# Kernel tuning notes

Hardware: AMD Instinct MI355X
Metric: run time of the kernel (lower is better)

The kernel has to match this reference:

```python
import jax, jax.numpy as jnp
import numpy as np

VOCAB, EMBED = 2048, 512
N = 65536  # = batch(2048) * num_slots(8) * tokens_per_slot(4)


def setup_inputs() -> dict:
    key = jax.random.key(0)
    ks = jax.random.split(key, 6)
    return {
        "z": jax.random.normal(ks[0], (N, 64), dtype=jnp.float32),
        "emb_W": jax.random.uniform(ks[1], (VOCAB, EMBED), dtype=jnp.float32,
                                    minval=-1.0 / VOCAB, maxval=1.0 / VOCAB),
        "pre_W": jax.random.normal(ks[2], (64, EMBED), dtype=jnp.float32) * 0.125,
        "pre_b": jax.random.normal(ks[3], (EMBED,), dtype=jnp.float32) * 0.02,
        "post_W": jax.random.normal(ks[4], (EMBED, 64), dtype=jnp.float32) * 0.044,
        "post_b": jax.random.normal(ks[5], (64,), dtype=jnp.float32) * 0.02,
    }


def reference(z, emb_W, pre_W, pre_b, post_W, post_b):
    # pre_quant_conv: Linear(64 -> embed_dim)
    zp = z @ pre_W + pre_b  # [N, E]
    # squared-distance to codebook: |z|^2 + |e|^2 - 2 z.e
    d = (jnp.sum(zp * zp, axis=1, keepdims=True)
         + jnp.sum(emb_W * emb_W, axis=1)
         - 2.0 * (zp @ emb_W.T))  # [N, V]
    tokens = jnp.argmin(d, axis=-1)  # [N] int
    z_q = emb_W[tokens]  # embedding gather [N, E]
    # post_quant_conv: Linear(embed_dim -> 64)
    z_q = z_q @ post_W + post_b  # [N, 64]
    return tokens, z_q
```

## Files before the change

### kernel.cpp

```cpp
#include <hip/hip_runtime.h>

#define EN  512
#define KIN 64
#define VN  2048
#define MARGIN 2.5e-3f
#define PRUNE  2.3e-3f
#define CAP 32

typedef __attribute__((ext_vector_type(8))) short bf16x8;
typedef __attribute__((ext_vector_type(4))) float f32x4;

static __device__ inline short f2bf(float f) {
  unsigned u = __builtin_bit_cast(unsigned, f);
  unsigned r = (u + 0x7FFFu + ((u >> 16) & 1u)) >> 16;
  return (short)r;
}
static __device__ inline unsigned encg(float f) {
  unsigned u = __builtin_bit_cast(unsigned, f);
  return (u & 0x80000000u) ? ~u : (u | 0x80000000u);
}
static __device__ inline float decg(unsigned e) {
  unsigned u = (e & 0x80000000u) ? (e & 0x7FFFFFFFu) : ~e;
  return __builtin_bit_cast(float, u);
}

__global__ __launch_bounds__(256) void k_prep(const float* __restrict__ emb,
                                              const float* __restrict__ pW,
                                              const float* __restrict__ pb,
                                              float* __restrict__ t2,
                                              short* __restrict__ dst,
                                              float* __restrict__ embq) {
#pragma clang fp contract(off)
  __shared__ float xs[64][129];
  const int tid = threadIdx.x;
  if (blockIdx.x >= 32) {
    const int gid = (blockIdx.x - 32) * 256 + tid;
    const int v = gid >> 6, c = gid & 63;
    const float* er = emb + (size_t)v * EN;
    float acc = 0.f;
#pragma unroll 8
    for (int k = 0; k < EN; ++k)
      acc = fmaf(er[k], pW[(size_t)k * 64 + c], acc);
    embq[(size_t)v * 64 + c] = acc + pb[c];
    return;
  }
  const int row0 = blockIdx.x * 64;
  float s[4];
  for (int ch = 0; ch < 4; ++ch) {
    __syncthreads();
#pragma unroll
    for (int i = 0; i < 32; ++i) {
      const int l = tid + i * 256;
      xs[l >> 7][l & 127] = emb[(size_t)(row0 + (l >> 7)) * EN + ch * 128 + (l & 127)];
    }
    __syncthreads();
    if (tid < 64) {
      float r8[8];
#pragma unroll
      for (int j = 0; j < 8; ++j) { const float v = xs[tid][j]; r8[j] = v * v; }
      for (int i = 8; i < 128; i += 8) {
#pragma unroll
        for (int j = 0; j < 8; ++j) { const float v = xs[tid][i + j]; r8[j] = r8[j] + v * v; }
      }
      s[ch] = ((r8[0] + r8[1]) + (r8[2] + r8[3])) + ((r8[4] + r8[5]) + (r8[6] + r8[7]));
    }
  }
  if (tid < 64) t2[row0 + tid] = (s[0] + s[1]) + (s[2] + s[3]);
  for (int i = tid; i < 64 * 64; i += 256) {
    const int v = row0 + (i >> 6), k8 = i & 63;
    const float4 f0 = ((const float4*)emb)[(size_t)v * 128 + k8 * 2];
    const float4 f1 = ((const float4*)emb)[(size_t)v * 128 + k8 * 2 + 1];
    short4 h0, h1;
    h0.x = f2bf(f0.x); h0.y = f2bf(f0.y); h0.z = f2bf(f0.z); h0.w = f2bf(f0.w);
    h1.x = f2bf(f1.x); h1.y = f2bf(f1.y); h1.z = f2bf(f1.z); h1.w = f2bf(f1.w);
    const int vt = v >> 4, vrow = v & 15, kb = k8 >> 2, q = k8 & 3;
    const int off = ((vt * 16 + kb) * 64 + q * 16 + vrow) * 8;
    *(short4*)&dst[off] = h0;
    *(short4*)&dst[off + 4] = h1;
  }
}

__global__ __launch_bounds__(512, 4) void k_dist(const float* __restrict__ z,
                                                 const float* __restrict__ preW,
                                                 const float* __restrict__ preb,
                                                 const short* __restrict__ embhs,
                                                 const float* __restrict__ embf,
                                                 const float* __restrict__ t2,
                                                 float* __restrict__ zp,
                                                 int* __restrict__ rowcnt,
                                                 unsigned short* __restrict__ slots,
                                                 float* __restrict__ gslots,
                                                 unsigned long long* __restrict__ keys) {
#pragma clang fp contract(off)
  __shared__ short As[64 * 512];
  __shared__ unsigned rmaxs[64];
  __shared__ int cnt_s[64];
  const int tid = threadIdx.x;
  const int wave = tid >> 6, lane = tid & 63;
  const int quad = lane >> 4, l15 = lane & 15;
  const int row0 = blockIdx.x * 64;

  if (tid < 64) { rmaxs[tid] = 0u; cnt_s[tid] = 0; keys[row0 + tid] = ~0ull; }

  {
    const int rg = tid >> 5, cg = tid & 31;
    for (int ph = 0; ph < 4; ++ph) {
      const int j = ph * 128 + 4 * cg;
      f32x4 acc[4];
#pragma unroll
      for (int r = 0; r < 4; ++r) acc[r] = (f32x4){0.f, 0.f, 0.f, 0.f};
#pragma unroll 4
      for (int k4 = 0; k4 < 16; ++k4) {
        f32x4 zr[4];
#pragma unroll
        for (int r = 0; r < 4; ++r)
          zr[r] = *(const f32x4*)&z[(size_t)(row0 + 4 * rg + r) * KIN + 4 * k4];
#pragma unroll
        for (int kk = 0; kk < 4; ++kk) {
          const f32x4 w = *(const f32x4*)&preW[(size_t)(4 * k4 + kk) * EN + j];
#pragma unroll
          for (int r = 0; r < 4; ++r) {
            acc[r][0] = fmaf(zr[r][kk], w[0], acc[r][0]);
            acc[r][1] = fmaf(zr[r][kk], w[1], acc[r][1]);
            acc[r][2] = fmaf(zr[r][kk], w[2], acc[r][2]);
            acc[r][3] = fmaf(zr[r][kk], w[3], acc[r][3]);
          }
        }
      }
      const f32x4 bb = *(const f32x4*)&preb[j];
      const int kb = j >> 5, q = (j >> 3) & 3, half = ((j >> 2) & 1) * 4;
#pragma unroll
      for (int r = 0; r < 4; ++r) {
        f32x4 o;
        o[0] = acc[r][0] + bb[0]; o[1] = acc[r][1] + bb[1];
        o[2] = acc[r][2] + bb[2]; o[3] = acc[r][3] + bb[3];
        const int row = 4 * rg + r;
        *(f32x4*)&zp[(size_t)(row0 + row) * EN + j] = o;
        short4 h;
        h.x = f2bf(o[0]); h.y = f2bf(o[1]); h.z = f2bf(o[2]); h.w = f2bf(o[3]);
        const int mt = row >> 4, mrow = row & 15;
        *(short4*)&As[((mt * 16 + kb) * 64 + q * 16 + mrow) * 8 + half] = h;
      }
    }
  }
  __syncthreads();

  for (int win = 0; win < 8; ++win) {
    const int v0 = win * 256 + wave * 32;
    const int vt0 = win * 16 + wave * 2;
    const short* B0 = embhs + (((size_t)vt0 * 16) * 64 + lane) * 8;
    const short* B1 = embhs + ((((size_t)vt0 + 1) * 16) * 64 + lane) * 8;
    const float t2v0 = t2[v0 + l15];
    const float t2v1 = t2[v0 + 16 + l15];
    f32x4 acc[4][2];
#pragma unroll
    for (int mt = 0; mt < 4; ++mt) {
      acc[mt][0] = (f32x4){0.f, 0.f, 0.f, 0.f};
      acc[mt][1] = (f32x4){0.f, 0.f, 0.f, 0.f};
    }
    bf16x8 b00 = *(const bf16x8*)&B0[0];
    bf16x8 b01 = *(const bf16x8*)&B1[0];
    bf16x8 b10 = *(const bf16x8*)&B0[512];
    bf16x8 b11 = *(const bf16x8*)&B1[512];
    for (int kb = 0; kb < 16; kb += 2) {
      const int k2 = (kb + 2) & 15;
      const bf16x8 n00 = *(const bf16x8*)&B0[k2 * 512];
      const bf16x8 n01 = *(const bf16x8*)&B1[k2 * 512];
      __builtin_amdgcn_s_setprio(1);
#pragma unroll
      for (int mt = 0; mt < 4; ++mt) {
        const bf16x8 a = *(const bf16x8*)&As[((mt * 16 + kb) * 64 + lane) * 8];
        acc[mt][0] = __builtin_amdgcn_mfma_f32_16x16x32_bf16(a, b00, acc[mt][0], 0, 0, 0);
        acc[mt][1] = __builtin_amdgcn_mfma_f32_16x16x32_bf16(a, b01, acc[mt][1], 0, 0, 0);
      }
      __builtin_amdgcn_s_setprio(0);
      const int k3 = (kb + 3) & 15;
      const bf16x8 n10 = *(const bf16x8*)&B0[k3 * 512];
      const bf16x8 n11 = *(const bf16x8*)&B1[k3 * 512];
      __builtin_amdgcn_s_setprio(1);
#pragma unroll
      for (int mt = 0; mt < 4; ++mt) {
        const bf16x8 a = *(const bf16x8*)&As[((mt * 16 + kb + 1) * 64 + lane) * 8];
        acc[mt][0] = __builtin_amdgcn_mfma_f32_16x16x32_bf16(a, b10, acc[mt][0], 0, 0, 0);
        acc[mt][1] = __builtin_amdgcn_mfma_f32_16x16x32_bf16(a, b11, acc[mt][1], 0, 0, 0);
      }
      __builtin_amdgcn_s_setprio(0);
      b00 = n00; b01 = n01; b10 = n10; b11 = n11;
    }

#pragma unroll
    for (int mt = 0; mt < 4; ++mt)
#pragma unroll
      for (int r = 0; r < 4; ++r) {
        acc[mt][0][r] = fmaf(2.f, acc[mt][0][r], -t2v0);
        acc[mt][1][r] = fmaf(2.f, acc[mt][1][r], -t2v1);
      }
#pragma unroll
    for (int mt = 0; mt < 4; ++mt)
#pragma unroll
      for (int r = 0; r < 4; ++r) {
        float m = fmaxf(acc[mt][0][r], acc[mt][1][r]);
        m = fmaxf(m, __shfl_xor(m, 1, 16));
        m = fmaxf(m, __shfl_xor(m, 2, 16));
        m = fmaxf(m, __shfl_xor(m, 4, 16));
        m = fmaxf(m, __shfl_xor(m, 8, 16));
        if (l15 == 0) atomicMax(&rmaxs[mt * 16 + quad * 4 + r], encg(m));
      }
#pragma unroll
    for (int mt = 0; mt < 4; ++mt)
#pragma unroll
      for (int r = 0; r < 4; ++r) {
        const int rl = mt * 16 + quad * 4 + r;
        const float thr = decg(rmaxs[rl]) - MARGIN;
        const int grow = row0 + rl;
#pragma unroll
        for (int nt = 0; nt < 2; ++nt) {
          const float gv = acc[mt][nt][r];
          if (gv > thr) {
            const int v = v0 + nt * 16 + l15;
            const int idx = atomicAdd(&cnt_s[rl], 1);
            if (idx < CAP) {
              slots[grow * CAP + idx] = (unsigned short)v;
              gslots[grow * CAP + idx] = gv;
            } else {
              float accx = 0.f;
              const float* zr = zp + (size_t)grow * EN;
              const float* er = embf + (size_t)v * EN;
              float r8n[8], sn[4];
#pragma unroll
              for (int ch = 0; ch < 4; ++ch) {
#pragma unroll
                for (int _j = 0; _j < 8; ++_j) r8n[_j] = 0.f;
#pragma unroll 8
                for (int kk = 0; kk < 128; ++kk) {
                  const int k = ch * 128 + kk;
                  const float zv = zr[k];
                  accx = fmaf(zv, er[k], accx);
                  r8n[kk & 7] = r8n[kk & 7] + zv * zv;
                }
                sn[ch] = ((r8n[0] + r8n[1]) + (r8n[2] + r8n[3])) + ((r8n[4] + r8n[5]) + (r8n[6] + r8n[7]));
              }
              const float t1v = (sn[0] + sn[1]) + (sn[2] + sn[3]);
              const float d = (t1v + t2[v]) - 2.0f * accx;
              atomicMin(keys + grow, ((unsigned long long)encg(d) << 32) | (unsigned)v);
            }
          }
        }
      }
  }
  __syncthreads();
  if (tid < 64) rowcnt[row0 + tid] = cnt_s[tid];
}

__global__ __launch_bounds__(256) void k_tail2(const float* __restrict__ zp,
                                               const float* __restrict__ embf,
                                               const float* __restrict__ t2,
                                               const int* __restrict__ rowcnt,
                                               const unsigned short* __restrict__ slots,
                                               const float* __restrict__ gslots,
                                               unsigned long long* __restrict__ keys,
                                               const float* __restrict__ embq,
                                               float* __restrict__ tokf,
                                               float* __restrict__ out) {
#pragma clang fp contract(off)
  __shared__ int toks[64];
  __shared__ float t1s[64];
  __shared__ int wl_n;
  __shared__ unsigned wl_s[64 * CAP];
  __shared__ __align__(16) unsigned short slot_l[64 * CAP];
  __shared__ __align__(16) float gslot_l[64 * CAP];
  __shared__ int rc_l[64];
  const int tid = threadIdx.x;
  const int wave = tid >> 6, lane = tid & 63;
  const int row0 = blockIdx.x * 64;
  if (tid == 0) wl_n = 0;
  {
    const uint4* sg = (const uint4*)(slots + (size_t)row0 * CAP);
    ((uint4*)slot_l)[tid] = sg[tid];
    const float4* gg = (const float4*)(gslots + (size_t)row0 * CAP);
    ((float4*)gslot_l)[tid] = gg[tid];
    ((float4*)gslot_l)[tid + 256] = gg[tid + 256];
    if (tid < 64) rc_l[tid] = rowcnt[row0 + tid];
  }
  __syncthreads();

  for (int rnd = 0; rnd < 16; ++rnd) {
    const int rl = wave * 16 + rnd;
    const int grow = row0 + rl;
    const int rc = rc_l[rl];
    const int cnt = min(rc, CAP);
    float g = -3.4e38f;
    int v = 0;
    if (lane < cnt) {
      v = slot_l[rl * CAP + lane];
      g = gslot_l[rl * CAP + lane];
    }
    float m = g;
#pragma unroll
    for (int s = 1; s < 64; s <<= 1) m = fmaxf(m, __shfl_xor(m, s, 64));
    const bool keep = (lane < cnt) && (g > m - PRUNE);
    const unsigned long long ball = __ballot(keep);
    const bool certified = (rc <= CAP) && (__popcll(ball) == 1);

    if (certified) {
      if (keep) toks[rl] = v;
      continue;
    }
    {
      const int ch = (lane >> 3) & 3;
      const int j = lane & 7;
      const float* zr = zp + (size_t)grow * EN + ch * 128 + j;
      float c;
      { const float x = zr[0]; c = x * x; }
#pragma unroll
      for (int t = 1; t < 16; ++t) { const float x = zr[8 * t]; c = c + x * x; }
      c = c + __shfl_xor(c, 1, 64);
      c = c + __shfl_xor(c, 2, 64);
      c = c + __shfl_xor(c, 4, 64);
      c = c + __shfl_xor(c, 8, 64);
      c = c + __shfl_xor(c, 16, 64);
      if (lane == 0) { t1s[rl] = c; toks[rl] = -1; }
    }
    const int nadd = __popcll(ball);
    int base = 0;
    if (lane == 0) base = atomicAdd(&wl_n, nadd);
    base = __shfl(base, 0, 64);
    if (keep) {
      const int pref = __popcll(ball & ((1ull << lane) - 1ull));
      wl_s[base + pref] = ((unsigned)rl << 11) | (unsigned)v;
    }
  }
  __syncthreads();

  const int n = wl_n;
  for (int i = tid; i < n; i += 256) {
    const unsigned e = wl_s[i];
    const int rl = (int)(e >> 11);
    const int v = (int)(e & 2047u);
    const float* zr = zp + (size_t)(row0 + rl) * EN;
    const float* er = embf + (size_t)v * EN;
    float acc = 0.f;
#pragma unroll 8
    for (int k4 = 0; k4 < 128; ++k4) {
      const float4 az = ((const float4*)zr)[k4];
      const float4 ee = ((const float4*)er)[k4];
      acc = fmaf(az.x, ee.x, acc); acc = fmaf(az.y, ee.y, acc);
      acc = fmaf(az.z, ee.z, acc); acc = fmaf(az.w, ee.w, acc);
    }
    const float d = (t1s[rl] + t2[v]) - 2.0f * acc;
    atomicMin(&keys[row0 + rl], ((unsigned long long)encg(d) << 32) | (unsigned)v);
  }
  __syncthreads();

  if (tid < 64) {
    int t = toks[tid];
    if (t < 0) {
      const unsigned long long kk = atomicAdd(&keys[row0 + tid], 0ull);
      t = (int)(unsigned)(kk & 0xFFFFFFFFull);
      toks[tid] = t;
    }
    tokf[row0 + tid] = (float)t;
  }
  __syncthreads();

  const float4* embq4 = (const float4*)embq;
  float4* out4 = (float4*)out;
  for (int i = tid; i < 64 * 16; i += 256) {
    const int rr = i >> 4, q = i & 15;
    out4[(size_t)(row0 + rr) * 16 + q] = embq4[(size_t)toks[rr] * 16 + q];
  }
}

extern "C" void kernel_launch(void* const* d_in, const int* in_sizes, int n_in,
                              void* d_out, int out_size, void* d_ws, size_t ws_size,
                              hipStream_t stream) {
  const float* z     = (const float*)d_in[0];
  const float* emb   = (const float*)d_in[1];
  const float* preW  = (const float*)d_in[2];
  const float* preb  = (const float*)d_in[3];
  const float* postW = (const float*)d_in[4];
  const float* postb = (const float*)d_in[5];
  const int N = in_sizes[0] / KIN;

  char* ws = (char*)d_ws;
  float* zp                = (float*)ws;
  unsigned long long* keys = (unsigned long long*)(ws + 134217728);
  float* t2                = (float*)(ws + 134742016);
  int* rowcnt              = (int*)(ws + 134750208);
  unsigned short* slots    = (unsigned short*)(ws + 135012352);
  float* gslots            = (float*)(ws + 139206656);
  short* embhs             = (short*)(ws + 147595264);
  float* embq              = (float*)(ws + 149692416);

  float* outf = (float*)d_out;

  k_prep  <<<32 + VN * 64 / 256, 256, 0, stream>>>(emb, postW, postb, t2, embhs, embq);
  k_dist  <<<N / 64,  512, 0, stream>>>(z, preW, preb, embhs, emb, t2,
                                        zp, rowcnt, slots, gslots, keys);
  k_tail2 <<<N / 64,  256, 0, stream>>>(zp, emb, t2, rowcnt, slots, gslots,
                                        keys, embq, outf, outf + N);
}
```

Baseline: 414.5 us.

## Fuse candidate refinement tail into distance kernel, keeping slots in LDS

Merges the k_tail2 refinement and output-gather stage into k_dist, so per-row candidate slots, scores and counts stay in shared memory instead of going through global buffers. This removes one kernel launch and the global round trip for slots, gslots and rowcnt. The worklist reuses the A-tile LDS region, and the loops are rescaled to 512 threads with 8 rows per wave. The cost is more LDS per block, which may reduce occupancy of the GEMM-heavy kernel, and the tail work now runs in the same block as the distance computation instead of overlapping with other blocks.

```diff
diff --git a/kernel.cpp b/kernel.cpp
--- a/kernel.cpp
+++ b/kernel.cpp
@@ -87,20 +87,26 @@
                                                  const float* __restrict__ embf,
                                                  const float* __restrict__ t2,
                                                  float* __restrict__ zp,
-                                                 int* __restrict__ rowcnt,
-                                                 unsigned short* __restrict__ slots,
-                                                 float* __restrict__ gslots,
-                                                 unsigned long long* __restrict__ keys) {
+                                                 unsigned long long* __restrict__ keys,
+                                                 const float* __restrict__ embq,
+                                                 float* __restrict__ tokf,
+                                                 float* __restrict__ out) {
 #pragma clang fp contract(off)
   __shared__ short As[64 * 512];
   __shared__ unsigned rmaxs[64];
   __shared__ int cnt_s[64];
+  __shared__ __align__(16) unsigned short slot_l[64 * CAP];
+  __shared__ __align__(16) float gslot_l[64 * CAP];
+  __shared__ int toks[64];
+  __shared__ float t1s[64];
+  __shared__ int wl_n;
   const int tid = threadIdx.x;
   const int wave = tid >> 6, lane = tid & 63;
   const int quad = lane >> 4, l15 = lane & 15;
   const int row0 = blockIdx.x * 64;
 
   if (tid < 64) { rmaxs[tid] = 0u; cnt_s[tid] = 0; keys[row0 + tid] = ~0ull; }
+  if (tid == 0) wl_n = 0;
 
   {
     const int rg = tid >> 5, cg = tid & 31;
@@ -220,8 +226,8 @@
             const int v = v0 + nt * 16 + l15;
             const int idx = atomicAdd(&cnt_s[rl], 1);
             if (idx < CAP) {
-              slots[grow * CAP + idx] = (unsigned short)v;
-              gslots[grow * CAP + idx] = gv;
+              slot_l[rl * CAP + idx] = (unsigned short)v;
+              gslot_l[rl * CAP + idx] = gv;
             } else {
               float accx = 0.f;
               const float* zr = zp + (size_t)grow * EN;
@@ -249,45 +255,13 @@
       }
   }
   __syncthreads();
-  if (tid < 64) rowcnt[row0 + tid] = cnt_s[tid];
-}
-
-__global__ __launch_bounds__(256) void k_tail2(const float* __restrict__ zp,
-                                               const float* __restrict__ embf,
-                                               const float* __restrict__ t2,
-                                               const int* __restrict__ rowcnt,
-                                               const unsigned short* __restrict__ slots,
-                                               const float* __restrict__ gslots,
-                                               unsigned long long* __restrict__ keys,
-                                               const float* __restrict__ embq,
-                                               float* __restrict__ tokf,
-                                               float* __restrict__ out) {
-#pragma clang fp contract(off)
-  __shared__ int toks[64];
-  __shared__ float t1s[64];
-  __shared__ int wl_n;
-  __shared__ unsigned wl_s[64 * CAP];
-  __shared__ __align__(16) unsigned short slot_l[64 * CAP];
-  __shared__ __align__(16) float gslot_l[64 * CAP];
-  __shared__ int rc_l[64];
-  const int tid = threadIdx.x;
-  const int wave = tid >> 6, lane = tid & 63;
-  const int row0 = blockIdx.x * 64;
-  if (tid == 0) wl_n = 0;
-  {
-    const uint4* sg = (const uint4*)(slots + (size_t)row0 * CAP);
-    ((uint4*)slot_l)[tid] = sg[tid];
-    const float4* gg = (const float4*)(gslots + (size_t)row0 * CAP);
-    ((float4*)gslot_l)[tid] = gg[tid];
-    ((float4*)gslot_l)[tid + 256] = gg[tid + 256];
-    if (tid < 64) rc_l[tid] = rowcnt[row0 + tid];
-  }
-  __syncthreads();
-
-  for (int rnd = 0; rnd < 16; ++rnd) {
-    const int rl = wave * 16 + rnd;
+
+  unsigned* wl_s = (unsigned*)As;
+
+  for (int rnd = 0; rnd < 8; ++rnd) {
+    const int rl = wave * 8 + rnd;
     const int grow = row0 + rl;
-    const int rc = rc_l[rl];
+    const int rc = cnt_s[rl];
     const int cnt = min(rc, CAP);
     float g = -3.4e38f;
     int v = 0;
@@ -333,7 +307,7 @@
   __syncthreads();
 
   const int n = wl_n;
-  for (int i = tid; i < n; i += 256) {
+  for (int i = tid; i < n; i += 512) {
     const unsigned e = wl_s[i];
     const int rl = (int)(e >> 11);
     const int v = (int)(e & 2047u);
@@ -365,7 +339,7 @@
 
   const float4* embq4 = (const float4*)embq;
   float4* out4 = (float4*)out;
-  for (int i = tid; i < 64 * 16; i += 256) {
+  for (int i = tid; i < 64 * 16; i += 512) {
     const int rr = i >> 4, q = i & 15;
     out4[(size_t)(row0 + rr) * 16 + q] = embq4[(size_t)toks[rr] * 16 + q];
   }
@@ -386,17 +360,12 @@
   float* zp                = (float*)ws;
   unsigned long long* keys = (unsigned long long*)(ws + 134217728);
   float* t2                = (float*)(ws + 134742016);
-  int* rowcnt              = (int*)(ws + 134750208);
-  unsigned short* slots    = (unsigned short*)(ws + 135012352);
-  float* gslots            = (float*)(ws + 139206656);
-  short* embhs             = (short*)(ws + 147595264);
-  float* embq              = (float*)(ws + 149692416);
+  short* embhs             = (short*)(ws + 134750208);
+  float* embq              = (float*)(ws + 136847360);
 
   float* outf = (float*)d_out;
 
-  k_prep  <<<32 + VN * 64 / 256, 256, 0, stream>>>(emb, postW, postb, t2, embhs, embq);
-  k_dist  <<<N / 64,  512, 0, stream>>>(z, preW, preb, embhs, emb, t2,
-                                        zp, rowcnt, slots, gslots, keys);
-  k_tail2 <<<N / 64,  256, 0, stream>>>(zp, emb, t2, rowcnt, slots, gslots,
-                                        keys, embq, outf, outf + N);
-}
+  k_prep<<<32 + VN * 64 / 256, 256, 0, stream>>>(emb, postW, postb, t2, embhs, embq);
+  k_dist<<<N / 64, 512, 0, stream>>>(z, preW, preb, embhs, emb, t2,
+                                     zp, keys, embq, outf, outf + N);
+}
```

Result: no change. 406.5 us (median of 2 runs) (-1.9%).
